# Kernel tuning notes

Measured on AMD Instinct MI355X. Metric: run time of the kernel, lower is better.

Reference implementation:

```python
import jax, jax.numpy as jnp
import numpy as np

P = 12              # output_size
SPATIAL_SCALE = 4.0  # feature stride; module divides roi coords by this
IMG = 800.0          # image-space extent for generated boxes


def setup_inputs() -> dict:
    key = jax.random.key(0)
    k1, k2, k3 = jax.random.split(key, 3)
    B, C, H, W = 2, 256, 200, 200
    x = jax.random.normal(k1, (B, C, H, W), dtype=jnp.float32)
    N = 1000
    b = jax.random.randint(k2, (N,), 0, B).astype(jnp.float32)
    c = jax.random.uniform(k3, (N, 4), minval=0.0, maxval=IMG - 8.0)
    x1 = jnp.minimum(c[:, 0], c[:, 1]); x2 = jnp.maximum(c[:, 0], c[:, 1]) + 8.0
    y1 = jnp.minimum(c[:, 2], c[:, 3]); y2 = jnp.maximum(c[:, 2], c[:, 3]) + 8.0
    rois = jnp.stack([b, x1, y1, x2, y2], axis=1)  # [N,5] (batch, x1, y1, x2, y2)
    return {"x": x, "rois": rois}


def _roi_align(x, rois):
    B, C, H, W = x.shape
    N = rois.shape[0]
    bidx = rois[:, 0].astype(jnp.int32)
    # map image-space coords to feature-space (module does rois /= spatial_scale)
    x1 = rois[:, 1] / SPATIAL_SCALE
    y1 = rois[:, 2] / SPATIAL_SCALE
    x2 = rois[:, 3] / SPATIAL_SCALE
    y2 = rois[:, 4] / SPATIAL_SCALE
    bin_h = (y2 - y1) / P
    bin_w = (x2 - x1) / P
    centers = jnp.arange(P, dtype=x.dtype) + 0.5
    ys = y1[:, None] + centers * bin_h[:, None]  # [N,P] sample rows (bin centers)
    xs = x1[:, None] + centers * bin_w[:, None]  # [N,P] sample cols
    ys = jnp.clip(ys, 0.0, H - 1)
    xs = jnp.clip(xs, 0.0, W - 1)
    y0f = jnp.floor(ys); x0f = jnp.floor(xs)
    ly = ys - y0f; lx = xs - x0f              # bilinear fractions
    y0 = y0f.astype(jnp.int32); x0 = x0f.astype(jnp.int32)
    y1i = jnp.minimum(y0 + 1, H - 1); x1i = jnp.minimum(x0 + 1, W - 1)
    # flatten feature map to [B*H*W, C] for single-index gathers (NHWC layout)
    feat = jnp.transpose(x, (0, 2, 3, 1)).reshape(B * H * W, C)
    base = bidx[:, None, None] * (H * W)

    def gather(yi, xi):
        idx = base + yi[:, :, None] * W + xi[:, None, :]  # [N,P,P]
        return feat[idx]                                   # [N,P,P,C]

    v00 = gather(y0, x0); v01 = gather(y0, x1i)
    v10 = gather(y1i, x0); v11 = gather(y1i, x1i)
    wy1 = ly[:, :, None, None]; wy0 = 1.0 - wy1
    wx1 = lx[:, None, :, None]; wx0 = 1.0 - wx1
    out = wy0 * wx0 * v00 + wy0 * wx1 * v01 + wy1 * wx0 * v10 + wy1 * wx1 * v11
    return jnp.transpose(out, (0, 3, 1, 2))  # [N, C, P, P]


def reference(x, rois):
    return _roi_align(x, rois)
```

## Files before the change

kernel.cpp:

```cpp
#include <hip/hip_runtime.h>
#include <hip/hip_bf16.h>

#define H_ 200
#define W_ 200
#define HW_ 40000
#define C_ 256
#define B_ 2
#define P_ 12
#define NBINS 144
#define CHUNK 32
#define TP 65

typedef float f32x4 __attribute__((ext_vector_type(4)));

__device__ __forceinline__ unsigned int bfbits(float f) {
  unsigned int u = __float_as_uint(f);
  return (u + 0x7FFFu + ((u >> 16) & 1u)) >> 16;
}
__device__ __forceinline__ float blo(unsigned int u) {
  return __uint_as_float(u << 16);
}
__device__ __forceinline__ float bhi(unsigned int u) {
  return __uint_as_float(u & 0xFFFF0000u);
}
__device__ __forceinline__ void nt_store4(float* p, float a, float b, float c,
                                          float d) {
  f32x4 v = {a, b, c, d};
  __builtin_nontemporal_store(v, reinterpret_cast<f32x4*>(p));
}

__global__ __launch_bounds__(256) void transpose_to_bf16_nhwc(
    const float* __restrict__ x, __hip_bfloat16* __restrict__ feat) {
  __shared__ float sT[64 * TP];
  const int t = threadIdx.x;
  const int p0 = blockIdx.x * 64;
  const int c0 = blockIdx.y * 64;
  const int b = blockIdx.z;

  const int px4 = (t & 15) * 4;
  const int cl = t >> 4;
#pragma unroll
  for (int pass = 0; pass < 4; ++pass) {
    const int c = pass * 16 + cl;
    const f32x4 v = __builtin_nontemporal_load(reinterpret_cast<const f32x4*>(
        x + (size_t)(b * C_ + c0 + c) * HW_ + p0 + px4));
    sT[(px4 + 0) * TP + c] = v.x;
    sT[(px4 + 1) * TP + c] = v.y;
    sT[(px4 + 2) * TP + c] = v.z;
    sT[(px4 + 3) * TP + c] = v.w;
  }
  __syncthreads();
  const int c8 = (t & 7) * 8;
  const int pxs = t >> 3;
#pragma unroll
  for (int pass = 0; pass < 2; ++pass) {
    const int px = pass * 32 + pxs;
    const float* r = &sT[px * TP + c8];
    uint4 w;
    w.x = bfbits(r[0]) | (bfbits(r[1]) << 16);
    w.y = bfbits(r[2]) | (bfbits(r[3]) << 16);
    w.z = bfbits(r[4]) | (bfbits(r[5]) << 16);
    w.w = bfbits(r[6]) | (bfbits(r[7]) << 16);
    *reinterpret_cast<uint4*>(feat + (size_t)(b * HW_ + p0 + px) * C_ + c0 +
                              c8) = w;
  }
}

__global__ __launch_bounds__(256, 6) void roi_gather_bf16(
    const __hip_bfloat16* __restrict__ feat, const float* __restrict__ rois,
    float* __restrict__ out, int N) {
  __shared__ float sw0[NBINS], sw1[NBINS], sw2[NBINS], sw3[NBINS];
  __shared__ int so0[NBINS], so1[NBINS], so2[NBINS], so3[NBINS];
  __shared__ float tile[2][CHUNK * TP];

  const int t = threadIdx.x;
  const int n = blockIdx.y;
  const int cbase = blockIdx.x * 64;
  if (n >= N) return;

  if (t < NBINS) {
    const int py = t / P_;
    const int px = t - py * P_;
    const float rx1 = rois[n * 5 + 1] * 0.25f;
    const float ry1 = rois[n * 5 + 2] * 0.25f;
    const float rx2 = rois[n * 5 + 3] * 0.25f;
    const float ry2 = rois[n * 5 + 4] * 0.25f;
    const int bi = (int)rois[n * 5 + 0];
    const float bh = (ry2 - ry1) * (1.0f / P_);
    const float bw = (rx2 - rx1) * (1.0f / P_);
    float ys = ry1 + ((float)py + 0.5f) * bh;
    float xs = rx1 + ((float)px + 0.5f) * bw;
    ys = fminf(fmaxf(ys, 0.0f), (float)(H_ - 1));
    xs = fminf(fmaxf(xs, 0.0f), (float)(W_ - 1));
    const float y0f = floorf(ys);
    const float x0f = floorf(xs);
    const float ly = ys - y0f;
    const float lx = xs - x0f;
    const int y0 = (int)y0f;
    const int x0 = (int)x0f;
    const int y1 = min(y0 + 1, H_ - 1);
    const int x1 = min(x0 + 1, W_ - 1);
    sw0[t] = (1.0f - ly) * (1.0f - lx);
    sw1[t] = (1.0f - ly) * lx;
    sw2[t] = ly * (1.0f - lx);
    sw3[t] = ly * lx;
    const int pb = bi * HW_;
    so0[t] = (pb + y0 * W_ + x0) * C_;
    so1[t] = (pb + y0 * W_ + x1) * C_;
    so2[t] = (pb + y1 * W_ + x0) * C_;
    so3[t] = (pb + y1 * W_ + x1) * C_;
  }
  __syncthreads();

  const int binq = t >> 3;
  const int c8 = (t & 7) * 8;
  const __hip_bfloat16* fb = feat + cbase;
  float* outn = out + ((size_t)n * C_ + cbase) * NBINS;

  for (int ch = 0; ch < 5; ++ch) {
    const int cs = (ch == 4) ? 16 : CHUNK;
    float* tb = tile[ch & 1];
    if (binq < cs) {
      const int bin = ch * CHUNK + binq;
      const uint4 a  = *reinterpret_cast<const uint4*>(fb + so0[bin] + c8);
      const uint4 b_ = *reinterpret_cast<const uint4*>(fb + so1[bin] + c8);
      const uint4 c_ = *reinterpret_cast<const uint4*>(fb + so2[bin] + c8);
      const uint4 d_ = *reinterpret_cast<const uint4*>(fb + so3[bin] + c8);
      const float w0 = sw0[bin], w1 = sw1[bin], w2 = sw2[bin], w3 = sw3[bin];
      float* tp = tb + binq * TP + c8;
      tp[0] = w0 * blo(a.x) + w1 * blo(b_.x) + w2 * blo(c_.x) + w3 * blo(d_.x);
      tp[1] = w0 * bhi(a.x) + w1 * bhi(b_.x) + w2 * bhi(c_.x) + w3 * bhi(d_.x);
      tp[2] = w0 * blo(a.y) + w1 * blo(b_.y) + w2 * blo(c_.y) + w3 * blo(d_.y);
      tp[3] = w0 * bhi(a.y) + w1 * bhi(b_.y) + w2 * bhi(c_.y) + w3 * bhi(d_.y);
      tp[4] = w0 * blo(a.z) + w1 * blo(b_.z) + w2 * blo(c_.z) + w3 * blo(d_.z);
      tp[5] = w0 * bhi(a.z) + w1 * bhi(b_.z) + w2 * bhi(c_.z) + w3 * bhi(d_.z);
      tp[6] = w0 * blo(a.w) + w1 * blo(b_.w) + w2 * blo(c_.w) + w3 * blo(d_.w);
      tp[7] = w0 * bhi(a.w) + w1 * bhi(b_.w) + w2 * bhi(c_.w) + w3 * bhi(d_.w);
    }
    __syncthreads();
    if (cs == CHUNK) {
#pragma unroll
      for (int r = 0; r < 2; ++r) {
        const int s = r * 256 + t;
        const int cc = s >> 3;
        const int q = s & 7;
        const float* tr = tb + cc;
        nt_store4(outn + (size_t)cc * NBINS + ch * CHUNK + 4 * q,
                  tr[(4 * q + 0) * TP], tr[(4 * q + 1) * TP],
                  tr[(4 * q + 2) * TP], tr[(4 * q + 3) * TP]);
      }
    } else {
      const int cc = t >> 2;
      const int q = t & 3;
      const float* tr = tb + cc;
      nt_store4(outn + (size_t)cc * NBINS + ch * CHUNK + 4 * q,
                tr[(4 * q + 0) * TP], tr[(4 * q + 1) * TP],
                tr[(4 * q + 2) * TP], tr[(4 * q + 3) * TP]);
    }
  }
}

__global__ void roi_naive_nchw(const float* __restrict__ x,
                               const float* __restrict__ rois,
                               float* __restrict__ out, int total) {
  const int gid = blockIdx.x * blockDim.x + threadIdx.x;
  if (gid >= total) return;
  const int bin = gid % NBINS;
  const int c   = (gid / NBINS) % C_;
  const int n   = gid / (NBINS * C_);
  const int py  = bin / P_;
  const int px  = bin - py * P_;
  const float rx1 = rois[n * 5 + 1] * 0.25f;
  const float ry1 = rois[n * 5 + 2] * 0.25f;
  const float rx2 = rois[n * 5 + 3] * 0.25f;
  const float ry2 = rois[n * 5 + 4] * 0.25f;
  const int bi = (int)rois[n * 5 + 0];
  const float bh = (ry2 - ry1) * (1.0f / P_);
  const float bw = (rx2 - rx1) * (1.0f / P_);
  float ys = fminf(fmaxf(ry1 + ((float)py + 0.5f) * bh, 0.0f), (float)(H_ - 1));
  float xs = fminf(fmaxf(rx1 + ((float)px + 0.5f) * bw, 0.0f), (float)(W_ - 1));
  const float y0f = floorf(ys), x0f = floorf(xs);
  const float ly = ys - y0f, lx = xs - x0f;
  const int y0 = (int)y0f, x0 = (int)x0f;
  const int y1 = min(y0 + 1, H_ - 1), x1 = min(x0 + 1, W_ - 1);
  const float* p = x + (size_t)(bi * C_ + c) * HW_;
  const float v = (1.0f - ly) * (1.0f - lx) * p[y0 * W_ + x0] +
                  (1.0f - ly) * lx * p[y0 * W_ + x1] +
                  ly * (1.0f - lx) * p[y1 * W_ + x0] +
                  ly * lx * p[y1 * W_ + x1];
  out[gid] = v;
}

extern "C" void kernel_launch(void* const* d_in, const int* in_sizes, int n_in,
                              void* d_out, int out_size, void* d_ws,
                              size_t ws_size, hipStream_t stream) {
  const float* x    = (const float*)d_in[0];
  const float* rois = (const float*)d_in[1];
  float* out = (float*)d_out;
  const int N = in_sizes[1] / 5;

  const size_t need = (size_t)B_ * C_ * HW_ * sizeof(__hip_bfloat16);
  if (ws_size >= need) {
    __hip_bfloat16* feat = (__hip_bfloat16*)d_ws;
    transpose_to_bf16_nhwc<<<dim3(HW_ / 64, C_ / 64, B_), 256, 0, stream>>>(
        x, feat);
    roi_gather_bf16<<<dim3(C_ / 64, N), 256, 0, stream>>>(feat, rois, out, N);
  } else {
    const int total = N * C_ * NBINS;
    roi_naive_nchw<<<dim3((total + 255) / 256), 256, 0, stream>>>(x, rois, out,
                                                                  total);
  }
}
```

Before: 72.50 us.

## Morton-sort ROIs and remap gather blocks per XCD for cache locality

Adds a single-block bitonic sort that orders ROIs by the Morton code of their centers. The gather kernel now uses a 1-D grid whose block IDs are remapped so that consecutive blocks landing on the same XCD process spatially adjacent ROIs and their four channel groups. The goal is more L2 reuse of the bf16 NHWC feature map within each XCD. The cost is an extra serial single-block kernel launch with many barriers, plus a workspace buffer for the permutation.

```diff
diff --git a/kernel.cpp b/kernel.cpp
--- a/kernel.cpp
+++ b/kernel.cpp
@@ -27,6 +27,53 @@
                                           float d) {
   f32x4 v = {a, b, c, d};
   __builtin_nontemporal_store(v, reinterpret_cast<f32x4*>(p));
+}
+
+__global__ __launch_bounds__(512) void morton_sort(
+    const float* __restrict__ rois, int N, unsigned int* __restrict__ perm) {
+  __shared__ unsigned int keys[1024];
+  const int t = threadIdx.x;
+  if (N > 1024) {
+    for (int i = t; i < N; i += 512) perm[i] = i;
+    return;
+  }
+  for (int i = t; i < 1024; i += 512) {
+    unsigned int v = 0xFFFFFFFFu;
+    if (i < N) {
+      const float cx = (rois[i * 5 + 1] + rois[i * 5 + 3]) * 0.125f;
+      const float cy = (rois[i * 5 + 2] + rois[i * 5 + 4]) * 0.125f;
+      unsigned int qx = (unsigned int)fminf(fmaxf(cx * 1.28f, 0.0f), 255.0f);
+      unsigned int qy = (unsigned int)fminf(fmaxf(cy * 1.28f, 0.0f), 255.0f);
+      unsigned int mx = qx, my = qy;
+      mx = (mx | (mx << 4)) & 0x0F0Fu;
+      mx = (mx | (mx << 2)) & 0x3333u;
+      mx = (mx | (mx << 1)) & 0x5555u;
+      my = (my | (my << 4)) & 0x0F0Fu;
+      my = (my | (my << 2)) & 0x3333u;
+      my = (my | (my << 1)) & 0x5555u;
+      v = (((mx | (my << 1)) << 10) | (unsigned int)i);
+    }
+    keys[i] = v;
+  }
+  __syncthreads();
+  for (int k = 2; k <= 1024; k <<= 1) {
+    for (int j = k >> 1; j > 0; j >>= 1) {
+      for (int i = t; i < 1024; i += 512) {
+        const int ixj = i ^ j;
+        if (ixj > i) {
+          const bool up = ((i & k) == 0);
+          const unsigned int a = keys[i];
+          const unsigned int b = keys[ixj];
+          if ((a > b) == up) {
+            keys[i] = b;
+            keys[ixj] = a;
+          }
+        }
+      }
+      __syncthreads();
+    }
+  }
+  for (int i = t; i < N; i += 512) perm[i] = keys[i] & 1023u;
 }
 
 __global__ __launch_bounds__(256) void transpose_to_bf16_nhwc(
@@ -68,16 +115,19 @@
 
 __global__ __launch_bounds__(256, 6) void roi_gather_bf16(
     const __hip_bfloat16* __restrict__ feat, const float* __restrict__ rois,
-    float* __restrict__ out, int N) {
+    const unsigned int* __restrict__ perm, float* __restrict__ out, int N,
+    int per_xcd) {
   __shared__ float sw0[NBINS], sw1[NBINS], sw2[NBINS], sw3[NBINS];
   __shared__ int so0[NBINS], so1[NBINS], so2[NBINS], so3[NBINS];
   __shared__ float tile[2][CHUNK * TP];
 
+  const int bid = blockIdx.x;
+  const int pos = (bid & 7) * per_xcd + (bid >> 3);
+  if (pos >= 4 * N) return;
+  const int n = (int)perm[pos >> 2];
+  const int cbase = (pos & 3) * 64;
+
   const int t = threadIdx.x;
-  const int n = blockIdx.y;
-  const int cbase = blockIdx.x * 64;
-  if (n >= N) return;
-
   if (t < NBINS) {
     const int py = t / P_;
     const int px = t - py * P_;
@@ -199,12 +249,18 @@
   float* out = (float*)d_out;
   const int N = in_sizes[1] / 5;
 
-  const size_t need = (size_t)B_ * C_ * HW_ * sizeof(__hip_bfloat16);
-  if (ws_size >= need) {
+  const size_t feat_bytes = (size_t)B_ * C_ * HW_ * sizeof(__hip_bfloat16);
+  const size_t perm_bytes = (size_t)((N > 1024) ? N : 1024) * sizeof(unsigned);
+  if (ws_size >= feat_bytes + perm_bytes) {
     __hip_bfloat16* feat = (__hip_bfloat16*)d_ws;
+    unsigned int* perm = (unsigned int*)((char*)d_ws + feat_bytes);
+    morton_sort<<<1, 512, 0, stream>>>(rois, N, perm);
     transpose_to_bf16_nhwc<<<dim3(HW_ / 64, C_ / 64, B_), 256, 0, stream>>>(
         x, feat);
-    roi_gather_bf16<<<dim3(C_ / 64, N), 256, 0, stream>>>(feat, rois, out, N);
+    const int total = 4 * N;
+    const int per_xcd = (total + 7) / 8;
+    roi_gather_bf16<<<dim3(8 * per_xcd), 256, 0, stream>>>(feat, rois, perm,
+                                                           out, N, per_xcd);
   } else {
     const int total = N * C_ * NBINS;
     roi_naive_nchw<<<dim3((total + 255) / 256), 256, 0, stream>>>(x, rois, out,
```

After: 97.13 us. 1.34x slower.
